# Optimization experiments

Hardware: AMD Instinct MI355X
Metric: run time of the kernel (lower is better)

The kernel has to match this reference:

```python
import jax, jax.numpy as jnp
import numpy as np

INPUT_SIZE = 512
HIDDEN_SIZE = 1024
OUTPUT_SIZE = 2
SEQ_LENGTH = 64
BATCH = 2048


def setup_inputs() -> dict:
    key = jax.random.key(0)
    ks = jax.random.split(key, 9)
    cin = INPUT_SIZE + HIDDEN_SIZE
    s = 1.0 / np.sqrt(cin)
    x = jax.random.normal(ks[0], (BATCH, SEQ_LENGTH, INPUT_SIZE), dtype=jnp.float32)
    Wf = jax.random.uniform(ks[1], (HIDDEN_SIZE, cin), jnp.float32, -s, s)
    bf = jax.random.uniform(ks[2], (HIDDEN_SIZE,), jnp.float32, -s, s)
    Wg = jax.random.uniform(ks[3], (HIDDEN_SIZE, cin), jnp.float32, -s, s)
    bg = jax.random.uniform(ks[4], (HIDDEN_SIZE,), jnp.float32, -s, s)
    Wh = jax.random.uniform(ks[5], (HIDDEN_SIZE, cin), jnp.float32, -s, s)
    bh = jax.random.uniform(ks[6], (HIDDEN_SIZE,), jnp.float32, -s, s)
    sf = 1.0 / np.sqrt(HIDDEN_SIZE)
    Wfc = jax.random.uniform(ks[7], (OUTPUT_SIZE, HIDDEN_SIZE), jnp.float32, -sf, sf)
    bfc = jax.random.uniform(ks[8], (OUTPUT_SIZE,), jnp.float32, -sf, sf)
    return {"x": x, "Wf": Wf, "bf": bf, "Wg": Wg, "bg": bg,
            "Wh": Wh, "bh": bh, "Wfc": Wfc, "bfc": bfc}


def _lnn_forward(x, Wf, bf, Wg, bg, Wh, bh, Wfc, bfc):
    B = x.shape[0]
    h0 = jnp.zeros((B, Wf.shape[0]), dtype=x.dtype)
    xs = jnp.swapaxes(x, 0, 1)  # [T, B, D]

    def step(h, xt):
        combined = jnp.concatenate([xt, h], axis=-1)  # [B, D+H]
        f_out = combined @ Wf.T + bf
        g_out = combined @ Wg.T + bg
        h_out = combined @ Wh.T + bh
        gate = jax.nn.sigmoid(-f_out)
        new_h = gate * g_out + (1.0 - gate) * h_out
        return new_h, None

    h_final, _ = jax.lax.scan(step, h0, xs)
    return h_final @ Wfc.T + bfc  # [B, output_size]


def reference(x, Wf, bf, Wg, bg, Wh, bh, Wfc, bfc):
    return _lnn_forward(x, Wf, bf, Wg, bg, Wh, bh, Wfc, bfc)
```

## Files before the change

### kernel.cpp

```cpp
#include <hip/hip_runtime.h>
#include <stdint.h>

#define BATCH 2048
#define TSEQ  64
#define DIN   512
#define HID   1024
#define CIN   1536

#define BM 128
#define BN 32
#define BK 64
#define KITERS (CIN / BK)

#define CHUNK   1088
#define A_CHUNKS 16
#define B_CHUNKS 4
#define A_BYTES (A_CHUNKS * CHUNK)
#define B_MAT   (B_CHUNKS * CHUNK)
#define B_BYTES (3 * B_MAT)

typedef __attribute__((ext_vector_type(8))) short bf16x8;
typedef __attribute__((ext_vector_type(4))) float f32x4;
typedef __attribute__((ext_vector_type(4))) float fvec4;
typedef __attribute__((ext_vector_type(4))) unsigned int uvec4;

__device__ __forceinline__ unsigned short f2bf(float f) {
    unsigned int u = __float_as_uint(f);
    u += 0x7fffu + ((u >> 16) & 1u);
    return (unsigned short)(u >> 16);
}
__device__ __forceinline__ float bf2f(unsigned short u) {
    return __uint_as_float(((unsigned int)u) << 16);
}

__device__ __forceinline__ void gload_lds16(const void* g, void* lds) {
    __builtin_amdgcn_global_load_lds(
        (const __attribute__((address_space(1))) void*)(uintptr_t)g,
        (__attribute__((address_space(3))) void*)(unsigned)(uintptr_t)lds,
        16, 0, 0);
}

__global__ __launch_bounds__(256) void convert_w(const float* __restrict__ Wf,
                                                 const float* __restrict__ Wg,
                                                 const float* __restrict__ Wh,
                                                 unsigned short* __restrict__ Wb) {
    int mat = blockIdx.y;
    const float* src = (mat == 0) ? Wf : ((mat == 1) ? Wg : Wh);
    size_t base = (size_t)mat * (size_t)(HID * CIN);
    size_t idx = ((size_t)blockIdx.x * 256 + threadIdx.x) * 8;
    const fvec4* s = (const fvec4*)(src + idx);
    fvec4 a = s[0], b = s[1];
    uvec4 o;
    o.x = (unsigned)f2bf(a.x) | ((unsigned)f2bf(a.y) << 16);
    o.y = (unsigned)f2bf(a.z) | ((unsigned)f2bf(a.w) << 16);
    o.z = (unsigned)f2bf(b.x) | ((unsigned)f2bf(b.y) << 16);
    o.w = (unsigned)f2bf(b.z) | ((unsigned)f2bf(b.w) << 16);
    *(uvec4*)(Wb + base + idx) = o;
}

__global__ __launch_bounds__(256) void convert_x(const float* __restrict__ x,
                                                 unsigned short* __restrict__ xb) {
    size_t e = ((size_t)blockIdx.x * 256 + threadIdx.x) * 8;
    int t   = (int)(e / ((size_t)BATCH * DIN));
    int rem = (int)(e % ((size_t)BATCH * DIN));
    int b = rem / DIN;
    int d = rem % DIN;
    const float* src = x + ((size_t)b * TSEQ + t) * DIN + d;
    fvec4 a = *(const fvec4*)src;
    fvec4 c = *(const fvec4*)(src + 4);
    uvec4 o;
    o.x = (unsigned)f2bf(a.x) | ((unsigned)f2bf(a.y) << 16);
    o.y = (unsigned)f2bf(a.z) | ((unsigned)f2bf(a.w) << 16);
    o.z = (unsigned)f2bf(c.x) | ((unsigned)f2bf(c.y) << 16);
    o.w = (unsigned)f2bf(c.z) | ((unsigned)f2bf(c.w) << 16);
    *(uvec4*)(xb + e) = o;
}

__global__ __launch_bounds__(256, 2) void step_kernel(
    const unsigned short* __restrict__ xb,
    const unsigned short* __restrict__ Wb,
    const float* __restrict__ bfv,
    const float* __restrict__ bgv,
    const float* __restrict__ bhv,
    const unsigned short* __restrict__ hin,
    unsigned short* __restrict__ hout,
    int t)
{
    __shared__ __align__(16) char ldsA[3][A_BYTES];
    __shared__ __align__(16) char ldsB[2][B_BYTES];

    const int tid  = threadIdx.x;
    const int bid  = blockIdx.x;
    const int n_tile = ((bid & 7) << 2) | ((bid >> 3) & 3);
    const int m_tile = bid >> 5;
    const int m0 = m_tile * BM;
    const int n0 = n_tile * BN;

    const int lane = tid & 63;
    const int wave = tid >> 6;
    const int wm = wave >> 1;
    const int wn = wave & 1;

    const int drow = lane >> 3;
    const int dcol = (lane & 7) * 8;

    f32x4 acc[3][4] = {};

    const int cg = n0 + wn * 16 + (lane & 15);
    const float biasF = bfv[cg];
    const float biasG = bgv[cg];
    const float biasH = bhv[cg];

    const unsigned short* xsrc = xb + (size_t)t * BATCH * DIN;

    int aoff[4];
#pragma unroll
    for (int mt = 0; mt < 4; ++mt) {
        int r = wm * 64 + mt * 16 + (lane & 15);
        aoff[mt] = (r >> 3) * CHUNK + (r & 7) * 128;
    }
    const int nloc = wn * 16 + (lane & 15);
    const int boff = (nloc >> 3) * CHUNK + (nloc & 7) * 128;
    const int kboff = (lane >> 4) * 16;

    auto stageA = [&](int ki, char* base) {
        const int k0 = ki * BK;
        const unsigned short* asrc;
        int astride;
        if (k0 < DIN) { asrc = xsrc + k0;        astride = DIN; }
        else          { asrc = hin + (k0 - DIN); astride = HID; }
#pragma unroll
        for (int c = 0; c < 4; ++c) {
            int chunk = wave * 4 + c;
            gload_lds16(asrc + (size_t)(m0 + chunk * 8 + drow) * astride + dcol,
                        base + chunk * CHUNK);
        }
    };
    auto stageB = [&](int ki, char* base) {
        const int k0 = ki * BK;
#pragma unroll
        for (int j = 0; j < 3; ++j) {
            int u = wave * 3 + j;
            int mat = u >> 2, chunk = u & 3;
            gload_lds16(Wb + (size_t)mat * (HID * CIN) + (size_t)(n0 + chunk * 8 + drow) * CIN
                           + k0 + dcol,
                        base + mat * B_MAT + chunk * CHUNK);
        }
    };
    auto compute = [&](const char* baseA, const char* baseB) {
#pragma unroll
        for (int ks = 0; ks < 2; ++ks) {
            const int kb = ks * 64 + kboff;
            bf16x8 af[4];
#pragma unroll
            for (int mt = 0; mt < 4; ++mt)
                af[mt] = *(const bf16x8*)(baseA + aoff[mt] + kb);
#pragma unroll
            for (int mat = 0; mat < 3; ++mat) {
                bf16x8 bq = *(const bf16x8*)(baseB + mat * B_MAT + boff + kb);
#pragma unroll
                for (int mt = 0; mt < 4; ++mt)
                    acc[mat][mt] = __builtin_amdgcn_mfma_f32_16x16x32_bf16(
                        af[mt], bq, acc[mat][mt], 0, 0, 0);
            }
        }
    };

    stageA(0, ldsA[0]);
    stageB(0, ldsB[0]);
    stageA(1, ldsA[1]);

#pragma unroll
    for (int p = 0; p < KITERS - 1; ++p) {
        asm volatile("s_waitcnt vmcnt(4) lgkmcnt(0)\n\ts_barrier" ::: "memory");
        stageB(p + 1, ldsB[(p + 1) & 1]);
        if (p + 2 < KITERS) stageA(p + 2, ldsA[(p + 2) % 3]);
        compute(ldsA[p % 3], ldsB[p & 1]);
    }
    asm volatile("s_waitcnt vmcnt(0) lgkmcnt(0)\n\ts_barrier" ::: "memory");
    compute(ldsA[(KITERS - 1) % 3], ldsB[(KITERS - 1) & 1]);

#pragma unroll
    for (int mt = 0; mt < 4; ++mt) {
        int rbase = m0 + wm * 64 + mt * 16 + (lane >> 4) * 4;
#pragma unroll
        for (int r = 0; r < 4; ++r) {
            float f  = acc[0][mt][r] + biasF;
            float g  = acc[1][mt][r] + biasG;
            float hh = acc[2][mt][r] + biasH;
            float gate = 1.0f / (1.0f + __expf(f));
            float nh = hh + gate * (g - hh);
            __builtin_nontemporal_store(f2bf(nh),
                hout + (size_t)(rbase + r) * HID + cg);
        }
    }
}

__global__ __launch_bounds__(256) void fc_kernel(const unsigned short* __restrict__ h,
                                                 const float* __restrict__ Wfc,
                                                 const float* __restrict__ bfc,
                                                 float* __restrict__ out) {
    int row = blockIdx.x;
    int tid = threadIdx.x;
    const unsigned short* hr = h + (size_t)row * HID;
    ushort4 hv = *(const ushort4*)(hr + tid * 4);
    float h0 = bf2f(hv.x), h1 = bf2f(hv.y), h2 = bf2f(hv.z), h3 = bf2f(hv.w);
    float4 w0 = *(const float4*)(Wfc + tid * 4);
    float4 w1 = *(const float4*)(Wfc + HID + tid * 4);
    float a0 = h0 * w0.x + h1 * w0.y + h2 * w0.z + h3 * w0.w;
    float a1 = h0 * w1.x + h1 * w1.y + h2 * w1.z + h3 * w1.w;
#pragma unroll
    for (int off = 32; off > 0; off >>= 1) {
        a0 += __shfl_down(a0, off);
        a1 += __shfl_down(a1, off);
    }
    __shared__ float red[2][4];
    if ((tid & 63) == 0) { red[0][tid >> 6] = a0; red[1][tid >> 6] = a1; }
    __syncthreads();
    if (tid == 0) out[(size_t)row * 2 + 0] = red[0][0] + red[0][1] + red[0][2] + red[0][3] + bfc[0];
    if (tid == 1) out[(size_t)row * 2 + 1] = red[1][0] + red[1][1] + red[1][2] + red[1][3] + bfc[1];
}

extern "C" void kernel_launch(void* const* d_in, const int* in_sizes, int n_in,
                              void* d_out, int out_size, void* d_ws, size_t ws_size,
                              hipStream_t stream) {
    const float* x   = (const float*)d_in[0];
    const float* Wf  = (const float*)d_in[1];
    const float* bfv = (const float*)d_in[2];
    const float* Wg  = (const float*)d_in[3];
    const float* bgv = (const float*)d_in[4];
    const float* Wh  = (const float*)d_in[5];
    const float* bhv = (const float*)d_in[6];
    const float* Wfc = (const float*)d_in[7];
    const float* bfc = (const float*)d_in[8];
    float* out = (float*)d_out;

    char* ws = (char*)d_ws;
    unsigned short* Wb = (unsigned short*)ws;
    size_t wb_bytes = (size_t)3 * HID * CIN * 2;
    size_t h_bytes  = (size_t)BATCH * HID * 2;
    unsigned short* h0 = (unsigned short*)(ws + wb_bytes);
    unsigned short* h1 = (unsigned short*)(ws + wb_bytes + h_bytes);
    unsigned short* xbuf = (unsigned short*)(ws + wb_bytes + 2 * h_bytes);

    convert_w<<<dim3(768, 3), 256, 0, stream>>>(Wf, Wg, Wh, Wb);
    convert_x<<<32768, 256, 0, stream>>>(x, xbuf);
    (void)hipMemsetAsync(h0, 0, h_bytes, stream);

    unsigned short* bufs[2] = {h0, h1};
    for (int t = 0; t < TSEQ; ++t) {
        step_kernel<<<512, 256, 0, stream>>>(xbuf, Wb, bfv, bgv, bhv,
                                             bufs[t & 1], bufs[(t + 1) & 1], t);
    }
    fc_kernel<<<BATCH, 256, 0, stream>>>(h0, Wfc, bfc, out);
}
```

Before: 1.874 ms.

## Split K across wave pairs instead of N, reduce partial sums via LDS

Each wave now covers both 16-column N subtiles but only half of every 64-wide K slice, where before it covered one N subtile over the full K slice. Each A fragment load now feeds twice as many MFMAs, which cuts LDS traffic for A per MFMA. The cost is a cross-wave reduction at the end: one wave of each pair writes its partial accumulators to LDS and the other adds them and runs the epilogue. The accumulator count doubles to 24 f32x4 per wave, which raises register pressure and may lower occupancy, and half the waves sit idle during the epilogue.

```diff
diff --git a/kernel.cpp b/kernel.cpp
--- a/kernel.cpp
+++ b/kernel.cpp
@@ -99,17 +99,21 @@
     const int lane = tid & 63;
     const int wave = tid >> 6;
     const int wm = wave >> 1;
-    const int wn = wave & 1;
+    const int kh = wave & 1;
 
     const int drow = lane >> 3;
     const int dcol = (lane & 7) * 8;
 
-    f32x4 acc[3][4] = {};
-
-    const int cg = n0 + wn * 16 + (lane & 15);
-    const float biasF = bfv[cg];
-    const float biasG = bgv[cg];
-    const float biasH = bhv[cg];
+    f32x4 acc[3][4][2] = {};
+
+    float biasF[2], biasG[2], biasH[2];
+#pragma unroll
+    for (int nt = 0; nt < 2; ++nt) {
+        int cgn = n0 + nt * 16 + (lane & 15);
+        biasF[nt] = bfv[cgn];
+        biasG[nt] = bgv[cgn];
+        biasH[nt] = bhv[cgn];
+    }
 
     const unsigned short* xsrc = xb + (size_t)t * BATCH * DIN;
 
@@ -119,9 +123,13 @@
         int r = wm * 64 + mt * 16 + (lane & 15);
         aoff[mt] = (r >> 3) * CHUNK + (r & 7) * 128;
     }
-    const int nloc = wn * 16 + (lane & 15);
-    const int boff = (nloc >> 3) * CHUNK + (nloc & 7) * 128;
-    const int kboff = (lane >> 4) * 16;
+    int boff[2];
+#pragma unroll
+    for (int nt = 0; nt < 2; ++nt) {
+        int nloc = nt * 16 + (lane & 15);
+        boff[nt] = (nloc >> 3) * CHUNK + (nloc & 7) * 128;
+    }
+    const int kb = kh * 64 + (lane >> 4) * 16;
 
     auto stageA = [&](int ki, char* base) {
         const int k0 = ki * BK;
@@ -148,22 +156,20 @@
         }
     };
     auto compute = [&](const char* baseA, const char* baseB) {
-#pragma unroll
-        for (int ks = 0; ks < 2; ++ks) {
-            const int kb = ks * 64 + kboff;
-            bf16x8 af[4];
-#pragma unroll
-            for (int mt = 0; mt < 4; ++mt)
-                af[mt] = *(const bf16x8*)(baseA + aoff[mt] + kb);
-#pragma unroll
-            for (int mat = 0; mat < 3; ++mat) {
-                bf16x8 bq = *(const bf16x8*)(baseB + mat * B_MAT + boff + kb);
+        bf16x8 af[4];
+#pragma unroll
+        for (int mt = 0; mt < 4; ++mt)
+            af[mt] = *(const bf16x8*)(baseA + aoff[mt] + kb);
+#pragma unroll
+        for (int mat = 0; mat < 3; ++mat)
+#pragma unroll
+            for (int nt = 0; nt < 2; ++nt) {
+                bf16x8 bq = *(const bf16x8*)(baseB + mat * B_MAT + boff[nt] + kb);
 #pragma unroll
                 for (int mt = 0; mt < 4; ++mt)
-                    acc[mat][mt] = __builtin_amdgcn_mfma_f32_16x16x32_bf16(
-                        af[mt], bq, acc[mat][mt], 0, 0, 0);
+                    acc[mat][mt][nt] = __builtin_amdgcn_mfma_f32_16x16x32_bf16(
+                        af[mt], bq, acc[mat][mt][nt], 0, 0, 0);
             }
-        }
     };
 
     stageA(0, ldsA[0]);
@@ -180,18 +186,46 @@
     asm volatile("s_waitcnt vmcnt(0) lgkmcnt(0)\n\ts_barrier" ::: "memory");
     compute(ldsA[(KITERS - 1) % 3], ldsB[(KITERS - 1) & 1]);
 
-#pragma unroll
-    for (int mt = 0; mt < 4; ++mt) {
-        int rbase = m0 + wm * 64 + mt * 16 + (lane >> 4) * 4;
-#pragma unroll
-        for (int r = 0; r < 4; ++r) {
-            float f  = acc[0][mt][r] + biasF;
-            float g  = acc[1][mt][r] + biasG;
-            float hh = acc[2][mt][r] + biasH;
-            float gate = 1.0f / (1.0f + __expf(f));
-            float nh = hh + gate * (g - hh);
-            __builtin_nontemporal_store(f2bf(nh),
-                hout + (size_t)(rbase + r) * HID + cg);
+    __syncthreads();
+    float* xch = (float*)&ldsA[0][0];
+    if (kh == 1) {
+        f32x4* dst = (f32x4*)xch + (size_t)wm * (24 * 64) + lane;
+#pragma unroll
+        for (int mat = 0; mat < 3; ++mat)
+#pragma unroll
+            for (int mt = 0; mt < 4; ++mt)
+#pragma unroll
+                for (int nt = 0; nt < 2; ++nt)
+                    dst[((mat * 4 + mt) * 2 + nt) * 64] = acc[mat][mt][nt];
+    }
+    __syncthreads();
+    if (kh == 0) {
+        const f32x4* src = (const f32x4*)xch + (size_t)wm * (24 * 64) + lane;
+#pragma unroll
+        for (int mat = 0; mat < 3; ++mat)
+#pragma unroll
+            for (int mt = 0; mt < 4; ++mt)
+#pragma unroll
+                for (int nt = 0; nt < 2; ++nt)
+                    acc[mat][mt][nt] += src[((mat * 4 + mt) * 2 + nt) * 64];
+
+#pragma unroll
+        for (int mt = 0; mt < 4; ++mt) {
+            int rbase = m0 + wm * 64 + mt * 16 + (lane >> 4) * 4;
+#pragma unroll
+            for (int nt = 0; nt < 2; ++nt) {
+                int cgn = n0 + nt * 16 + (lane & 15);
+#pragma unroll
+                for (int r = 0; r < 4; ++r) {
+                    float f  = acc[0][mt][nt][r] + biasF[nt];
+                    float g  = acc[1][mt][nt][r] + biasG[nt];
+                    float hh = acc[2][mt][nt][r] + biasH[nt];
+                    float gate = 1.0f / (1.0f + __expf(f));
+                    float nh = hh + gate * (g - hh);
+                    __builtin_nontemporal_store(f2bf(nh),
+                        hout + (size_t)(rbase + r) * HID + cgn);
+                }
+            }
         }
     }
 }
```

Result: slower. 1.991 ms (+6.2%).
